# Performance work log

Measured on AMD Instinct MI355X. Metric: run time of the kernel, lower is better.

The kernel has to match this reference:

```python
import jax, jax.numpy as jnp
import numpy as np

N = 14        # nodes per graph (fixed by hidden*14 in the Linear)
H = 4         # attention heads
F_IN = 128    # num_feature
C = 64        # hidden (per-head out_channels; concat=False -> mean over heads)
NEG_SLOPE = 0.2  # PyG GATConv default negative_slope


def gat_conv(x, src, dst, W, a_src, a_dst, b):
    """One PyG-style GATConv on a single graph.
    x: [N, F]  W: [F, H*C]  a_src/a_dst: [H, C]  b: [C]
    src/dst: [E] int (self-loops already appended). concat=False -> mean over heads.
    """
    h = (x @ W).reshape(N, H, C)                       # [N,H,C]
    al_src = jnp.einsum('nhc,hc->nh', h, a_src)        # [N,H]
    al_dst = jnp.einsum('nhc,hc->nh', h, a_dst)        # [N,H]
    e = jax.nn.leaky_relu(al_src[src] + al_dst[dst], NEG_SLOPE)  # [E,H]
    # softmax over incoming edges of each destination node (stable)
    m = jax.ops.segment_max(e, dst, num_segments=N)    # [N,H]
    ex = jnp.exp(e - m[dst])
    denom = jax.ops.segment_sum(ex, dst, num_segments=N)
    alpha = ex / denom[dst]                            # [E,H]
    out = jax.ops.segment_sum(alpha[:, :, None] * h[src], dst, num_segments=N)  # [N,H,C]
    return out.mean(axis=1) + b                        # [N,C]


def setup_inputs() -> dict:
    key = jax.random.key(0)
    ks = jax.random.split(key, 12)
    B, E = 16384, 182
    feature = jax.random.normal(ks[0], (B, N, F_IN), dtype=jnp.float32)
    edge_list = jax.random.randint(ks[1], (B, E, 2), 0, N, dtype=jnp.int64)

    def glorot(k, shape):
        fan = shape[0] + shape[-1]
        return jax.random.normal(k, shape, dtype=jnp.float32) * jnp.sqrt(2.0 / fan)

    return {
        'feature': feature,
        'edge_list': edge_list,
        'W1': glorot(ks[2], (F_IN, H * C)),
        'a_src1': glorot(ks[3], (H, C)),
        'a_dst1': glorot(ks[4], (H, C)),
        'b1': jnp.zeros((C,), jnp.float32),
        'W2': glorot(ks[5], (C, H * C)),
        'a_src2': glorot(ks[6], (H, C)),
        'a_dst2': glorot(ks[7], (H, C)),
        'b2': jnp.zeros((C,), jnp.float32),
        'W_lin': glorot(ks[8], (N * C, C // 2)),
        'b_lin': jnp.zeros((C // 2,), jnp.float32),
        'W_pred': glorot(ks[9], (C // 2, 1)),
        'b_pred': jnp.zeros((1,), jnp.float32),
    }


def reference(feature, edge_list, W1, a_src1, a_dst1, b1, W2, a_src2, a_dst2, b2,
              W_lin, b_lin, W_pred, b_pred):
    B = feature.shape[0]
    # PyG GATConv adds self-loops by default
    loops = jnp.broadcast_to(jnp.arange(N, dtype=edge_list.dtype), (B, N))
    src = jnp.concatenate([edge_list[..., 0], loops], axis=1)  # [B, E+N]
    dst = jnp.concatenate([edge_list[..., 1], loops], axis=1)

    def per_graph(x, s, d):
        h = jax.nn.relu(gat_conv(x, s, d, W1, a_src1, a_dst1, b1))
        # dropout is identity in eval mode
        h = gat_conv(h, s, d, W2, a_src2, a_dst2, b2)       # [N,C]
        z = h.reshape(-1) @ W_lin + b_lin                    # [C//2]
        p = z @ W_pred + b_pred                              # [1]
        return jax.nn.sigmoid(p)

    return jax.vmap(per_graph)(feature, src, dst)            # [B,1]
```

## Files before the change

### kernel.cpp

```cpp
#include <hip/hip_runtime.h>

#define NN 14
#define HH 4
#define CC 64
#define FF 128
#define EE 182

typedef __attribute__((ext_vector_type(8))) short bf16x8;
typedef __attribute__((ext_vector_type(4))) float f32x4;
typedef __attribute__((ext_vector_type(4))) unsigned u32x4;

__device__ __forceinline__ unsigned f2bf(float f) {
    unsigned u = __float_as_uint(f);
    return (u + 0x7fffu + ((u >> 16) & 1u)) >> 16;
}
__device__ __forceinline__ bf16x8 mk8(unsigned a, unsigned b, unsigned c, unsigned d) {
    u32x4 u = {a, b, c, d};
    return __builtin_bit_cast(bf16x8, u);
}

__global__ void prep_pack(const float* __restrict__ W1, const float* __restrict__ W2,
                          const float* __restrict__ Wl, const float* __restrict__ Wpred,
                          const float* __restrict__ bl, const float* __restrict__ bp,
                          const float* __restrict__ as1, const float* __restrict__ ad1,
                          const float* __restrict__ as2, const float* __restrict__ ad2,
                          short* __restrict__ wp1, short* __restrict__ wp2,
                          short* __restrict__ battn1, short* __restrict__ battn2,
                          float* __restrict__ wcomb) {
    int gid = blockIdx.x * 256 + threadIdx.x;
    if (gid < 32768) {
        int j = gid & 7, L = (gid >> 3) & 63, kk = (gid >> 9) & 3, nt = gid >> 11;
        int k = kk * 32 + (L >> 4) * 8 + j, n = nt * 16 + (L & 15);
        wp1[gid] = (short)f2bf(W1[k * 256 + n]);
    } else if (gid < 49152) {
        int g2 = gid - 32768;
        int j = g2 & 7, L = (g2 >> 3) & 63, kk = (g2 >> 9) & 1, nt = g2 >> 10;
        int k = kk * 32 + (L >> 4) * 8 + j, n = nt * 16 + (L & 15);
        wp2[g2] = (short)f2bf(W2[k * 256 + n]);
    } else if (gid < 51200) {
        int g2 = gid - 49152;
        int j = g2 & 7, L = (g2 >> 3) & 63, kk = g2 >> 9;
        int n = L & 15, k = kk * 32 + (L >> 4) * 8 + j;
        float val = 0.f;
        if (n < 8) {
            const float* av = ((n >> 2) ? ad1 : as1) + (n & 3) * 64;
            const float* wr = W1 + k * 256 + (n & 3) * 64;
            for (int c = 0; c < 64; ++c) val += wr[c] * av[c];
        }
        battn1[g2] = (short)f2bf(val);
    } else if (gid < 52224) {
        int g2 = gid - 51200;
        int j = g2 & 7, L = (g2 >> 3) & 63, kk = g2 >> 9;
        int n = L & 15, k = kk * 32 + (L >> 4) * 8 + j;
        float val = 0.f;
        if (n < 8) {
            const float* av = ((n >> 2) ? ad2 : as2) + (n & 3) * 64;
            const float* wr = W2 + k * 256 + (n & 3) * 64;
            for (int c = 0; c < 64; ++c) val += wr[c] * av[c];
        }
        battn2[g2] = (short)f2bf(val);
    } else if (gid < 53120) {
        int i = gid - 52224;
        const float* wr = Wl + i * 32;
        float acc = 0.f;
        #pragma unroll
        for (int j = 0; j < 32; ++j) acc += wr[j] * Wpred[j];
        wcomb[i] = acc;
    } else if (gid == 53120) {
        float acc = bp[0];
        #pragma unroll
        for (int j = 0; j < 32; ++j) acc += bl[j] * Wpred[j];
        wcomb[896] = acc;
    }
}

template<int KK, bool RELU>
__device__ __forceinline__ void gat_layer(int lane,
    const bf16x8* a, const short* wpB,
    const float* __restrict__ bias,
    const unsigned* cnt, const float* alsd,
    f32x4* o, unsigned (*po)[2])
{
    const int m = lane & 15, q = lane >> 4;
    f32x4 agg[4];
    #pragma unroll
    for (int ct = 0; ct < 4; ++ct) agg[ct] = f32x4{0.f, 0.f, 0.f, 0.f};

    #pragma unroll
    for (int hp = 0; hp < 2; ++hp) {
        unsigned hb[8][2];
        #pragma unroll
        for (int hsub = 0; hsub < 2; ++hsub) {
            f32x4 c[4];
            #pragma unroll
            for (int ct = 0; ct < 4; ++ct) c[ct] = f32x4{0.f, 0.f, 0.f, 0.f};
            #pragma unroll
            for (int ct = 0; ct < 4; ++ct)
                #pragma unroll
                for (int kk = 0; kk < KK; ++kk) {
                    bf16x8 b = *(const bf16x8*)(wpB +
                        ((((hp * 2 + hsub) * 4 + ct) * KK + kk) * 64 + lane) * 8);
                    c[ct] = __builtin_amdgcn_mfma_f32_16x16x32_bf16(a[kk], b, c[ct], 0, 0, 0);
                }
            #pragma unroll
            for (int ct = 0; ct < 4; ++ct) {
                hb[hsub * 4 + ct][0] = f2bf(c[ct][0]) | (f2bf(c[ct][1]) << 16);
                hb[hsub * 4 + ct][1] = f2bf(c[ct][2]) | (f2bf(c[ct][3]) << 16);
            }
        }

        const int hh = hp * 2 + (q >> 1);
        const float myald = alsd[64 + hh * 16 + m];
        float v[8], s8 = 0.f;
        #pragma unroll
        for (int j = 0; j < 8; ++j) {
            int s = (q & 1) * 8 + j;
            float l = alsd[hh * 16 + s] + myald;
            l = (l > 0.f) ? l : 0.2f * l;
            float e = __expf(l) * (float)cnt[s * 16 + m];
            v[j] = e; s8 += e;
        }
        s8 += __shfl_xor(s8, 16);
        float inv = (s8 > 0.f) ? 0.25f / s8 : 0.f;
        unsigned pb[4];
        #pragma unroll
        for (int j2 = 0; j2 < 4; ++j2)
            pb[j2] = f2bf(v[2 * j2] * inv) | (f2bf(v[2 * j2 + 1] * inv) << 16);
        bf16x8 P = mk8(pb[0], pb[1], pb[2], pb[3]);

        #pragma unroll
        for (int ct = 0; ct < 4; ++ct) {
            unsigned aw[4];
            #pragma unroll
            for (int jj = 0; jj < 4; ++jj) {
                int srcl = ((q & 1) * 2 + (jj >> 1)) * 16 + m;
                unsigned aE = __shfl((int)hb[ct][jj & 1], srcl);
                unsigned aO = __shfl((int)hb[4 + ct][jj & 1], srcl);
                aw[jj] = (q >> 1) ? aO : aE;
            }
            agg[ct] = __builtin_amdgcn_mfma_f32_16x16x32_bf16(
                mk8(aw[0], aw[1], aw[2], aw[3]), P, agg[ct], 0, 0, 0);
        }
    }

    #pragma unroll
    for (int ct = 0; ct < 4; ++ct) {
        float4 bb = *(const float4*)(bias + ct * 16 + q * 4);
        float o0 = agg[ct][0] + bb.x, o1 = agg[ct][1] + bb.y;
        float o2 = agg[ct][2] + bb.z, o3 = agg[ct][3] + bb.w;
        if (RELU) {
            o0 = fmaxf(o0, 0.f); o1 = fmaxf(o1, 0.f);
            o2 = fmaxf(o2, 0.f); o3 = fmaxf(o3, 0.f);
            if (m >= NN) { o0 = 0.f; o1 = 0.f; o2 = 0.f; o3 = 0.f; }
            po[ct][0] = f2bf(o0) | (f2bf(o1) << 16);
            po[ct][1] = f2bf(o2) | (f2bf(o3) << 16);
        } else {
            o[ct] = f32x4{o0, o1, o2, o3};
        }
    }
}

__global__ __launch_bounds__(512, 4) void gat_fused(
    const float* __restrict__ feature,
    const int*   __restrict__ edge_list,
    const float* __restrict__ b1, const float* __restrict__ b2,
    const short* __restrict__ wp1,
    const short* __restrict__ wpck,
    const float* __restrict__ wcomb,
    float* __restrict__ out, int B)
{
    const int w = threadIdx.x >> 6, lane = threadIdx.x & 63;
    const int g = blockIdx.x * 8 + w;
    const int m = lane & 15, q = lane >> 4;

    __shared__ __align__(16) short swts[19456];
    __shared__ unsigned slab[8 * 384];

    {
        const u32x4* srcw = (const u32x4*)wpck;
        u32x4* dstw = (u32x4*)swts;
        #pragma unroll
        for (int r = 0; r < 5; ++r) {
            int i = r * 512 + threadIdx.x;
            if (i < 2432) dstw[i] = srcw[i];
        }
    }
    __syncthreads();
    if (g >= B) return;

    const short* swp2  = swts;
    const short* sbat1 = swts + 16384;
    const short* sbat2 = swts + 18432;
    unsigned* cnt  = slab + w * 384;
    float*    alsd = (float*)(slab + w * 384 + 256);

    #pragma unroll
    for (int i = 0; i < 4; ++i) cnt[i * 64 + lane] = 0u;
    const int2* ep = (const int2*)edge_list + (size_t)g * EE;
    #pragma unroll
    for (int r = 0; r < 3; ++r) {
        int i = r * 64 + lane;
        if (i < EE) { int2 e = ep[i]; atomicAdd(&cnt[e.x * 16 + e.y], 1u); }
    }
    if (lane < NN) atomicAdd(&cnt[lane * 17], 1u);

    const float* xg = feature + (size_t)g * (NN * FF) + m * FF;
    bf16x8 a1[4];
    #pragma unroll
    for (int kk = 0; kk < 4; ++kk) {
        if (m < NN) {
            float4 v0 = *(const float4*)(xg + kk * 32 + q * 8);
            float4 v1 = *(const float4*)(xg + kk * 32 + q * 8 + 4);
            a1[kk] = mk8(f2bf(v0.x) | (f2bf(v0.y) << 16), f2bf(v0.z) | (f2bf(v0.w) << 16),
                         f2bf(v1.x) | (f2bf(v1.y) << 16), f2bf(v1.z) | (f2bf(v1.w) << 16));
        } else a1[kk] = mk8(0, 0, 0, 0);
    }

    {
        f32x4 ca = f32x4{0.f, 0.f, 0.f, 0.f};
        #pragma unroll
        for (int kk = 0; kk < 4; ++kk) {
            bf16x8 b = *(const bf16x8*)(sbat1 + (kk * 64 + lane) * 8);
            ca = __builtin_amdgcn_mfma_f32_16x16x32_bf16(a1[kk], b, ca, 0, 0, 0);
        }
        if (m < 8) *(f32x4*)(alsd + (m >> 2) * 64 + (m & 3) * 16 + q * 4) = ca;
    }

    unsigned po1[4][2];
    gat_layer<4, true>(lane, a1, wp1, b1, cnt, alsd, nullptr, po1);

    bf16x8 a2[2];
    #pragma unroll
    for (int kk = 0; kk < 2; ++kk) {
        unsigned wv[4];
        #pragma unroll
        for (int j2 = 0; j2 < 4; ++j2) {
            int srcl = ((q & 1) * 2 + (j2 >> 1)) * 16 + m;
            unsigned vE = __shfl((int)po1[2 * kk][j2 & 1], srcl);
            unsigned vO = __shfl((int)po1[2 * kk + 1][j2 & 1], srcl);
            wv[j2] = (q >> 1) ? vO : vE;
        }
        a2[kk] = mk8(wv[0], wv[1], wv[2], wv[3]);
    }

    {
        f32x4 ca = f32x4{0.f, 0.f, 0.f, 0.f};
        #pragma unroll
        for (int kk = 0; kk < 2; ++kk) {
            bf16x8 b = *(const bf16x8*)(sbat2 + (kk * 64 + lane) * 8);
            ca = __builtin_amdgcn_mfma_f32_16x16x32_bf16(a2[kk], b, ca, 0, 0, 0);
        }
        if (m < 8) *(f32x4*)(alsd + (m >> 2) * 64 + (m & 3) * 16 + q * 4) = ca;
    }

    f32x4 o2[4];
    gat_layer<2, false>(lane, a2, swp2, b2, cnt, alsd, o2, nullptr);

    float p = 0.f;
    if (m < NN) {
        const float* wc = wcomb + m * 64 + q * 4;
        #pragma unroll
        for (int ct = 0; ct < 4; ++ct) {
            float4 w4 = *(const float4*)(wc + ct * 16);
            p += o2[ct][0] * w4.x + o2[ct][1] * w4.y +
                 o2[ct][2] * w4.z + o2[ct][3] * w4.w;
        }
    }
    p += __shfl_xor(p, 1);  p += __shfl_xor(p, 2);  p += __shfl_xor(p, 4);
    p += __shfl_xor(p, 8);  p += __shfl_xor(p, 16); p += __shfl_xor(p, 32);
    if (lane == 0) out[g] = 1.f / (1.f + __expf(-(p + wcomb[896])));
}

extern "C" void kernel_launch(void* const* d_in, const int* in_sizes, int n_in,
                              void* d_out, int out_size, void* d_ws, size_t ws_size,
                              hipStream_t stream) {
    const float* feature = (const float*)d_in[0];
    const int*   edges   = (const int*)d_in[1];
    const float* W1  = (const float*)d_in[2];
    const float* as1 = (const float*)d_in[3];
    const float* ad1 = (const float*)d_in[4];
    const float* b1  = (const float*)d_in[5];
    const float* W2  = (const float*)d_in[6];
    const float* as2 = (const float*)d_in[7];
    const float* ad2 = (const float*)d_in[8];
    const float* b2  = (const float*)d_in[9];
    const float* Wl  = (const float*)d_in[10];
    const float* bl  = (const float*)d_in[11];
    const float* Wp  = (const float*)d_in[12];
    const float* bp  = (const float*)d_in[13];
    float* out = (float*)d_out;

    short* wp1    = (short*)d_ws;
    short* wp2    = wp1 + 32768;
    short* battn1 = wp2 + 16384;
    short* battn2 = battn1 + 2048;
    float* wcomb  = (float*)(battn2 + 1024);

    prep_pack<<<208, 256, 0, stream>>>(W1, W2, Wl, Wp, bl, bp, as1, ad1, as2, ad2,
                                       wp1, wp2, battn1, battn2, wcomb);

    const int B = in_sizes[0] / (NN * FF);
    gat_fused<<<(B + 7) / 8, 512, 0, stream>>>(feature, edges, b1, b2,
                                               wp1, wp2, wcomb, out, B);
}
```

Before: 286.2 us.

## Overlap edge/feature loads with weight staging, transpose float edge counts, cheaper bf16 pack

```diff
diff --git a/kernel.cpp b/kernel.cpp
--- a/kernel.cpp
+++ b/kernel.cpp
@@ -13,6 +13,10 @@
 __device__ __forceinline__ unsigned f2bf(float f) {
     unsigned u = __float_as_uint(f);
     return (u + 0x7fffu + ((u >> 16) & 1u)) >> 16;
+}
+__device__ __forceinline__ unsigned pack2bf(float lo, float hi) {
+    return __builtin_amdgcn_perm(__float_as_uint(hi) + 0x8000u,
+                                 __float_as_uint(lo) + 0x8000u, 0x07060302u);
 }
 __device__ __forceinline__ bf16x8 mk8(unsigned a, unsigned b, unsigned c, unsigned d) {
     u32x4 u = {a, b, c, d};
@@ -78,7 +82,7 @@
 __device__ __forceinline__ void gat_layer(int lane,
     const bf16x8* a, const short* wpB,
     const float* __restrict__ bias,
-    const unsigned* cnt, const float* alsd,
+    const float* cntf, const float* alsd,
     f32x4* o, unsigned (*po)[2])
 {
     const int m = lane & 15, q = lane >> 4;
@@ -104,29 +108,29 @@
                 }
             #pragma unroll
             for (int ct = 0; ct < 4; ++ct) {
-                hb[hsub * 4 + ct][0] = f2bf(c[ct][0]) | (f2bf(c[ct][1]) << 16);
-                hb[hsub * 4 + ct][1] = f2bf(c[ct][2]) | (f2bf(c[ct][3]) << 16);
+                hb[hsub * 4 + ct][0] = pack2bf(c[ct][0], c[ct][1]);
+                hb[hsub * 4 + ct][1] = pack2bf(c[ct][2], c[ct][3]);
             }
         }
 
         const int hh = hp * 2 + (q >> 1);
         const float myald = alsd[64 + hh * 16 + m];
+        const float* asrc = alsd + hh * 16 + (q & 1) * 8;
+        const float* csrc = cntf + m * 20 + (q & 1) * 8;
+        f32x4 aL = *(const f32x4*)asrc, aH = *(const f32x4*)(asrc + 4);
+        f32x4 cL = *(const f32x4*)csrc, cH = *(const f32x4*)(csrc + 4);
         float v[8], s8 = 0.f;
         #pragma unroll
         for (int j = 0; j < 8; ++j) {
-            int s = (q & 1) * 8 + j;
-            float l = alsd[hh * 16 + s] + myald;
-            l = (l > 0.f) ? l : 0.2f * l;
-            float e = __expf(l) * (float)cnt[s * 16 + m];
+            float l = ((j < 4) ? aL[j] : aH[j - 4]) + myald;
+            l = fmaxf(l, 0.f) + 0.2f * fminf(l, 0.f);
+            float e = __expf(l) * ((j < 4) ? cL[j] : cH[j - 4]);
             v[j] = e; s8 += e;
         }
         s8 += __shfl_xor(s8, 16);
         float inv = (s8 > 0.f) ? 0.25f / s8 : 0.f;
-        unsigned pb[4];
-        #pragma unroll
-        for (int j2 = 0; j2 < 4; ++j2)
-            pb[j2] = f2bf(v[2 * j2] * inv) | (f2bf(v[2 * j2 + 1] * inv) << 16);
-        bf16x8 P = mk8(pb[0], pb[1], pb[2], pb[3]);
+        bf16x8 P = mk8(pack2bf(v[0] * inv, v[1] * inv), pack2bf(v[2] * inv, v[3] * inv),
+                       pack2bf(v[4] * inv, v[5] * inv), pack2bf(v[6] * inv, v[7] * inv));
 
         #pragma unroll
         for (int ct = 0; ct < 4; ++ct) {
@@ -152,8 +156,8 @@
             o0 = fmaxf(o0, 0.f); o1 = fmaxf(o1, 0.f);
             o2 = fmaxf(o2, 0.f); o3 = fmaxf(o3, 0.f);
             if (m >= NN) { o0 = 0.f; o1 = 0.f; o2 = 0.f; o3 = 0.f; }
-            po[ct][0] = f2bf(o0) | (f2bf(o1) << 16);
-            po[ct][1] = f2bf(o2) | (f2bf(o3) << 16);
+            po[ct][0] = pack2bf(o0, o1);
+            po[ct][1] = pack2bf(o2, o3);
         } else {
             o[ct] = f32x4{o0, o1, o2, o3};
         }
@@ -174,47 +178,53 @@
     const int m = lane & 15, q = lane >> 4;
 
     __shared__ __align__(16) short swts[19456];
-    __shared__ unsigned slab[8 * 384];
-
-    {
-        const u32x4* srcw = (const u32x4*)wpck;
-        u32x4* dstw = (u32x4*)swts;
-        #pragma unroll
-        for (int r = 0; r < 5; ++r) {
-            int i = r * 512 + threadIdx.x;
-            if (i < 2432) dstw[i] = srcw[i];
-        }
-    }
+    __shared__ __align__(16) unsigned slab[8 * 448];
+
+    float* cntf = (float*)(slab + w * 448);
+    float* alsd = (float*)(slab + w * 448 + 320);
+
+    const bool live = (g < B);
+
+    const u32x4* srcw = (const u32x4*)wpck;
+    u32x4* dstw = (u32x4*)swts;
+    #pragma unroll
+    for (int r = 0; r < 5; ++r) {
+        int i = r * 512 + threadIdx.x;
+        if (i < 2432) dstw[i] = srcw[i];
+    }
+
+    #pragma unroll
+    for (int i = 0; i < 5; ++i) cntf[i * 64 + lane] = 0.f;
+    if (live) {
+        const int2* ep = (const int2*)edge_list + (size_t)g * EE;
+        #pragma unroll
+        for (int r = 0; r < 3; ++r) {
+            int i = r * 64 + lane;
+            if (i < EE) { int2 e = ep[i]; atomicAdd(&cntf[e.y * 20 + e.x], 1.f); }
+        }
+        if (lane < NN) atomicAdd(&cntf[lane * 21], 1.f);
+    }
+
+    bf16x8 a1[4];
+    #pragma unroll
+    for (int kk = 0; kk < 4; ++kk) a1[kk] = mk8(0, 0, 0, 0);
+    if (live && m < NN) {
+        const float* xg = feature + (size_t)g * (NN * FF) + m * FF;
+        #pragma unroll
+        for (int kk = 0; kk < 4; ++kk) {
+            float4 v0 = *(const float4*)(xg + kk * 32 + q * 8);
+            float4 v1 = *(const float4*)(xg + kk * 32 + q * 8 + 4);
+            a1[kk] = mk8(pack2bf(v0.x, v0.y), pack2bf(v0.z, v0.w),
+                         pack2bf(v1.x, v1.y), pack2bf(v1.z, v1.w));
+        }
+    }
+
     __syncthreads();
-    if (g >= B) return;
+    if (!live) return;
 
     const short* swp2  = swts;
     const short* sbat1 = swts + 16384;
     const short* sbat2 = swts + 18432;
-    unsigned* cnt  = slab + w * 384;
-    float*    alsd = (float*)(slab + w * 384 + 256);
-
-    #pragma unroll
-    for (int i = 0; i < 4; ++i) cnt[i * 64 + lane] = 0u;
-    const int2* ep = (const int2*)edge_list + (size_t)g * EE;
-    #pragma unroll
-    for (int r = 0; r < 3; ++r) {
-        int i = r * 64 + lane;
-        if (i < EE) { int2 e = ep[i]; atomicAdd(&cnt[e.x * 16 + e.y], 1u); }
-    }
-    if (lane < NN) atomicAdd(&cnt[lane * 17], 1u);
-
-    const float* xg = feature + (size_t)g * (NN * FF) + m * FF;
-    bf16x8 a1[4];
-    #pragma unroll
-    for (int kk = 0; kk < 4; ++kk) {
-        if (m < NN) {
-            float4 v0 = *(const float4*)(xg + kk * 32 + q * 8);
-            float4 v1 = *(const float4*)(xg + kk * 32 + q * 8 + 4);
-            a1[kk] = mk8(f2bf(v0.x) | (f2bf(v0.y) << 16), f2bf(v0.z) | (f2bf(v0.w) << 16),
-                         f2bf(v1.x) | (f2bf(v1.y) << 16), f2bf(v1.z) | (f2bf(v1.w) << 16));
-        } else a1[kk] = mk8(0, 0, 0, 0);
-    }
 
     {
         f32x4 ca = f32x4{0.f, 0.f, 0.f, 0.f};
@@ -227,7 +237,7 @@
     }
 
     unsigned po1[4][2];
-    gat_layer<4, true>(lane, a1, wp1, b1, cnt, alsd, nullptr, po1);
+    gat_layer<4, true>(lane, a1, wp1, b1, cntf, alsd, nullptr, po1);
 
     bf16x8 a2[2];
     #pragma unroll
@@ -254,7 +264,7 @@
     }
 
     f32x4 o2[4];
-    gat_layer<2, false>(lane, a2, swp2, b2, cnt, alsd, o2, nullptr);
+    gat_layer<2, false>(lane, a2, swp2, b2, cntf, alsd, o2, nullptr);
 
     float p = 0.f;
     if (m < NN) {
```

Measured after the change: 281.4 us. Within noise of the previous version (-1.7%).
